# Performance work log

Measured on AMD Instinct MI355X. Metric: run time of the kernel, lower is better.

## Reference

```python
import jax, jax.numpy as jnp
import numpy as np

B, S, D, F, K = 32, 512, 256, 256, 3

def setup_inputs() -> dict:
    key = jax.random.key(0)
    ks = jax.random.split(key, 8)
    x = jax.random.normal(ks[0], (B, S, D), dtype=jnp.float32)
    target = jax.random.uniform(ks[1], (B, S), dtype=jnp.float32, minval=1.0, maxval=8.0)
    expand_max_len = int(jnp.round(target.sum(-1)).max())
    sc = 0.05
    conv1_w = jax.random.normal(ks[2], (F, D, K), dtype=jnp.float32) * sc
    conv1_b = jnp.zeros((F,), jnp.float32)
    conv2_w = jax.random.normal(ks[3], (F, F, K), dtype=jnp.float32) * sc
    conv2_b = jnp.zeros((F,), jnp.float32)
    norm1_g = jnp.ones((F,), jnp.float32); norm1_b = jnp.zeros((F,), jnp.float32)
    norm2_g = jnp.ones((F,), jnp.float32); norm2_b = jnp.zeros((F,), jnp.float32)
    lin_w = jax.random.normal(ks[4], (F,), dtype=jnp.float32) * sc
    lin_b = jnp.zeros((), jnp.float32)
    return {"x": x, "target": target, "conv1_w": conv1_w, "conv1_b": conv1_b,
            "conv2_w": conv2_w, "conv2_b": conv2_b, "norm1_g": norm1_g, "norm1_b": norm1_b,
            "norm2_g": norm2_g, "norm2_b": norm2_b, "lin_w": lin_w, "lin_b": lin_b,
            "expand_max_len": expand_max_len}

def _layernorm(h, g, b, eps=1e-5):
    mu = jnp.mean(h, axis=-1, keepdims=True)
    var = jnp.mean((h - mu) ** 2, axis=-1, keepdims=True)
    return (h - mu) * jax.lax.rsqrt(var + eps) * g + b

def _conv1d(h_bsd, w, bias):
    # h_bsd: [B,S,C] -> conv over time with 'same' padding -> [B,S,F]
    h = jnp.transpose(h_bsd, (0, 2, 1))  # [B,C,S]
    out = jax.lax.conv_general_dilated(h, w, window_strides=(1,),
                                       padding=[(K // 2, K // 2)],
                                       dimension_numbers=("NCH", "OIH", "NCH"))
    out = out + bias[None, :, None]
    return jnp.transpose(out, (0, 2, 1))  # [B,S,F]

def _duration_predict(x, conv1_w, conv1_b, conv2_w, conv2_b,
                      norm1_g, norm1_b, norm2_g, norm2_b, lin_w, lin_b):
    h = _conv1d(x, conv1_w, conv1_b)
    h = jax.nn.relu(_layernorm(h, norm1_g, norm1_b))  # dropout is identity in eval
    h = _conv1d(h, conv2_w, conv2_b)
    h = jax.nn.relu(_layernorm(h, norm2_g, norm2_b))
    return jax.nn.relu(h @ lin_w + lin_b)  # [B,S]

def _length_regulate(x, target, L):
    d = jnp.round(target)                # [B,S] integer-valued durations
    ends = jnp.cumsum(d, axis=-1)        # [B,S]
    starts = ends - d
    t = jnp.arange(L, dtype=d.dtype)     # [L]
    mask = ((t[None, None, :] >= starts[:, :, None]) &
            (t[None, None, :] < ends[:, :, None])).astype(x.dtype)  # [B,S,L]
    # x^T @ mask -> [B,D,L]; return transposed [B,L,D]
    return jnp.einsum("bsd,bsl->bld", x, mask)

def reference(x, target, conv1_w, conv1_b, conv2_w, conv2_b,
              norm1_g, norm1_b, norm2_g, norm2_b, lin_w, lin_b, expand_max_len):
    predicted_len = _duration_predict(x, conv1_w, conv1_b, conv2_w, conv2_b,
                                      norm1_g, norm1_b, norm2_g, norm2_b, lin_w, lin_b)
    output = _length_regulate(x, target, expand_max_len)
    return (output, predicted_len)
```

## Files before the change

### kernel.cpp

```cpp
#include <hip/hip_runtime.h>
#include <hip/hip_bf16.h>

#define NB 32
#define NS 512
#define NC 256
#define NKSTEP 24
#define ROWS 32
#define HALO_ROWS 34

typedef __attribute__((ext_vector_type(8))) short short8;
typedef __attribute__((ext_vector_type(4))) float f32x4;

__device__ __forceinline__ unsigned pack2(float a, float b) {
    __hip_bfloat16 ha = __float2bfloat16(a), hb = __float2bfloat16(b);
    return ((unsigned)(*(unsigned short*)&hb) << 16) | (unsigned)(*(unsigned short*)&ha);
}

__global__ __launch_bounds__(256) void prep_w(const float* __restrict__ w,
                                              unsigned short* __restrict__ Bp) {
    const int f = blockIdx.x, t = threadIdx.x;
    const float* wf = w + (size_t)f * 768 + t * 3;
    const float v[3] = {wf[0], wf[1], wf[2]};
#pragma unroll
    for (int shift = 0; shift < 3; ++shift) {
        const int k = shift * 256 + t;
        const int o = f * 32 + (k >> 5) * 8192 + (k & 31);
        __hip_bfloat16 h = __float2bfloat16(v[shift]);
        Bp[o] = *(unsigned short*)&h;
    }
}

template <bool FINAL, typename Tin>
__global__ __launch_bounds__(256, 2) void conv_mfma(
    const Tin* __restrict__ in,
    const uint4* __restrict__ Bp,
    const float* __restrict__ bias,
    const float* __restrict__ gamma,
    const float* __restrict__ beta,
    const float* __restrict__ linw,
    const float* __restrict__ linb,
    void* __restrict__ outp)
{
    __shared__ __align__(16) uint4 xs[HALO_ROWS * 32];
    __shared__ float red[ROWS][4][2];
    __shared__ float dotb[ROWS][4];

    const int tid = threadIdx.x;
    const int b   = blockIdx.x >> 4;
    const int s0  = (blockIdx.x & 15) << 5;

    {
        const int slot = tid & 31;
        for (int r = tid >> 5; r < HALO_ROWS; r += 8) {
            const int s = s0 - 1 + r;
            uint4 v = {0u, 0u, 0u, 0u};
            if (s >= 0 && s < NS) {
                if constexpr (sizeof(Tin) == 4) {
                    const float* src = (const float*)in + ((size_t)(b * NS + s)) * NC + slot * 8;
                    const float4 lo = *(const float4*)src;
                    const float4 hi = *(const float4*)(src + 4);
                    v.x = pack2(lo.x, lo.y); v.y = pack2(lo.z, lo.w);
                    v.z = pack2(hi.x, hi.y); v.w = pack2(hi.z, hi.w);
                } else {
                    v = *(const uint4*)((const unsigned short*)in +
                                        ((size_t)(b * NS + s)) * NC + slot * 8);
                }
            }
            xs[r * 32 + (slot ^ ((r & 7) << 2))] = v;
        }
    }
    __syncthreads();

    const int lane = tid & 63;
    const int w    = tid >> 6;
    const int n0   = w << 6;
    const int l15  = lane & 15;
    const int lg   = lane >> 4;

    f32x4 acc[2][4];
#pragma unroll
    for (int mi = 0; mi < 2; ++mi)
#pragma unroll
        for (int ni = 0; ni < 4; ++ni) acc[mi][ni] = (f32x4){0.f, 0.f, 0.f, 0.f};

    const uint4* bbase = Bp + (size_t)(n0 + l15) * 4 + lg;

    auto lda = [&](int ks, int mi) -> short8 {
        const int row  = mi * 16 + l15 + (ks >> 3);
        int slot = ((ks & 7) << 2) + lg;
        slot ^= (row & 7) << 2;
        return *(const short8*)&xs[row * 32 + slot];
    };
    auto ldb = [&](int ks, int ni) -> short8 {
        return *(const short8*)(const void*)(bbase + ks * 1024 + ni * 64);
    };

    short8 a0[2], b0[4], a1[2], b1[4];
#pragma unroll
    for (int mi = 0; mi < 2; ++mi) a0[mi] = lda(0, mi);
#pragma unroll
    for (int ni = 0; ni < 4; ++ni) b0[ni] = ldb(0, ni);

    for (int ks = 0; ks < NKSTEP; ks += 2) {
#pragma unroll
        for (int ni = 0; ni < 4; ++ni) b1[ni] = ldb(ks + 1, ni);
#pragma unroll
        for (int mi = 0; mi < 2; ++mi) a1[mi] = lda(ks + 1, mi);
#pragma unroll
        for (int mi = 0; mi < 2; ++mi)
#pragma unroll
            for (int ni = 0; ni < 4; ++ni)
                acc[mi][ni] = __builtin_amdgcn_mfma_f32_16x16x32_bf16(
                    a0[mi], b0[ni], acc[mi][ni], 0, 0, 0);
        if (ks + 2 < NKSTEP) {
#pragma unroll
            for (int ni = 0; ni < 4; ++ni) b0[ni] = ldb(ks + 2, ni);
#pragma unroll
            for (int mi = 0; mi < 2; ++mi) a0[mi] = lda(ks + 2, mi);
        }
#pragma unroll
        for (int mi = 0; mi < 2; ++mi)
#pragma unroll
            for (int ni = 0; ni < 4; ++ni)
                acc[mi][ni] = __builtin_amdgcn_mfma_f32_16x16x32_bf16(
                    a1[mi], b1[ni], acc[mi][ni], 0, 0, 0);
    }

    float bv[4], gv[4], bt[4], lwv[4];
#pragma unroll
    for (int ni = 0; ni < 4; ++ni) {
        const int col = n0 + ni * 16 + l15;
        bv[ni] = bias[col]; gv[ni] = gamma[col]; bt[ni] = beta[col];
        if constexpr (FINAL) lwv[ni] = linw[col];
    }
#pragma unroll
    for (int mi = 0; mi < 2; ++mi)
#pragma unroll
        for (int ni = 0; ni < 4; ++ni)
#pragma unroll
            for (int i = 0; i < 4; ++i) acc[mi][ni][i] += bv[ni];

#pragma unroll
    for (int mi = 0; mi < 2; ++mi) {
        float s[4] = {0, 0, 0, 0}, q[4] = {0, 0, 0, 0};
#pragma unroll
        for (int ni = 0; ni < 4; ++ni)
#pragma unroll
            for (int i = 0; i < 4; ++i) {
                const float v = acc[mi][ni][i];
                s[i] += v; q[i] += v * v;
            }
#pragma unroll
        for (int i = 0; i < 4; ++i)
#pragma unroll
            for (int m = 1; m < 16; m <<= 1) {
                s[i] += __shfl_xor(s[i], m, 64);
                q[i] += __shfl_xor(q[i], m, 64);
            }
        if (l15 == 0) {
#pragma unroll
            for (int i = 0; i < 4; ++i) {
                red[mi * 16 + lg * 4 + i][w][0] = s[i];
                red[mi * 16 + lg * 4 + i][w][1] = q[i];
            }
        }
    }
    __syncthreads();

#pragma unroll
    for (int mi = 0; mi < 2; ++mi) {
#pragma unroll
        for (int i = 0; i < 4; ++i) {
            const int row = mi * 16 + lg * 4 + i;
            float sum = 0.f, sq = 0.f;
#pragma unroll
            for (int ww = 0; ww < 4; ++ww) { sum += red[row][ww][0]; sq += red[row][ww][1]; }
            const float mu = sum * (1.f / 256.f);
            const float rs = rsqrtf(sq * (1.f / 256.f) - mu * mu + 1e-5f);
            float p = 0.f;
#pragma unroll
            for (int ni = 0; ni < 4; ++ni) {
                const float y = fmaxf(0.f, (acc[mi][ni][i] - mu) * rs * gv[ni] + bt[ni]);
                if constexpr (!FINAL) {
                    __hip_bfloat16 h = __float2bfloat16(y);
                    ((unsigned short*)outp)[((size_t)(b * NS + s0 + row)) * NC +
                                            n0 + ni * 16 + l15] = *(unsigned short*)&h;
                } else {
                    p += y * lwv[ni];
                }
            }
            if constexpr (FINAL) {
#pragma unroll
                for (int m = 1; m < 16; m <<= 1) p += __shfl_xor(p, m, 64);
                if (l15 == 0) dotb[row][w] = p;
            }
        }
    }
    if constexpr (FINAL) {
        __syncthreads();
        if (tid < ROWS) {
            const float tot = dotb[tid][0] + dotb[tid][1] + dotb[tid][2] + dotb[tid][3] + linb[0];
            ((float*)outp)[b * NS + s0 + tid] = fmaxf(0.f, tot);
        }
    }
}

__global__ __launch_bounds__(256) void scan_kernel(const float* __restrict__ target,
                                                   float* __restrict__ ends)
{
    __shared__ float bufa[512], bufb[512];
    const int b = blockIdx.x, t = threadIdx.x;
    const float* tb = target + (size_t)b * NS;
    bufa[t]       = rintf(tb[t]);
    bufa[t + 256] = rintf(tb[t + 256]);
    __syncthreads();
    float* src = bufa;
    float* dst = bufb;
    for (int off = 1; off < 512; off <<= 1) {
        for (int i = t; i < 512; i += 256) {
            float v = src[i];
            if (i >= off) v += src[i - off];
            dst[i] = v;
        }
        __syncthreads();
        float* tmp = src; src = dst; dst = tmp;
    }
    ends[(size_t)b * NS + t]       = src[t];
    ends[(size_t)b * NS + t + 256] = src[t + 256];
}

__global__ __launch_bounds__(256) void gather_kernel(const float* __restrict__ x,
                                                     const float* __restrict__ ends,
                                                     float* __restrict__ out, int L)
{
    const int b   = blockIdx.y;
    const int t0  = blockIdx.x * 8;
    const int tid = threadIdx.x;
    const float* eb = ends + (size_t)b * NS;
    const float total = eb[511];
    for (int i = 0; i < 8; ++i) {
        const int t = t0 + i;
        if (t >= L) return;
        const float tf = (float)t;
        float v = 0.f;
        if (tf < total) {
            int pos = 0;
#pragma unroll
            for (int st = 256; st > 0; st >>= 1)
                if (eb[pos + st - 1] <= tf) pos += st;
            v = x[((size_t)(b * NS + pos)) * NC + tid];
        }
        out[((size_t)b * L + t) * NC + tid] = v;
    }
}

extern "C" void kernel_launch(void* const* d_in, const int* in_sizes, int n_in,
                              void* d_out, int out_size, void* d_ws, size_t ws_size,
                              hipStream_t stream)
{
    const float* x    = (const float*)d_in[0];
    const float* targ = (const float*)d_in[1];
    const float* c1w  = (const float*)d_in[2];
    const float* c1b  = (const float*)d_in[3];
    const float* c2w  = (const float*)d_in[4];
    const float* c2b  = (const float*)d_in[5];
    const float* n1g  = (const float*)d_in[6];
    const float* n1b  = (const float*)d_in[7];
    const float* n2g  = (const float*)d_in[8];
    const float* n2b  = (const float*)d_in[9];
    const float* lw   = (const float*)d_in[10];
    const float* lb   = (const float*)d_in[11];

    const int L = (out_size - NB * NS) / (NB * NC);

    unsigned short* Bp1 = (unsigned short*)d_ws;
    unsigned short* Bp2 = Bp1 + 196608;
    unsigned short* h1  = Bp2 + 196608;
    float* ends = (float*)(h1 + (size_t)NB * NS * NC);
    float* out  = (float*)d_out;
    float* pred = out + (size_t)NB * (size_t)L * NC;

    prep_w<<<dim3(256), 256, 0, stream>>>(c1w, Bp1);
    prep_w<<<dim3(256), 256, 0, stream>>>(c2w, Bp2);

    conv_mfma<false, float><<<dim3(NB * 16), 256, 0, stream>>>(
        x, (const uint4*)Bp1, c1b, n1g, n1b, nullptr, nullptr, (void*)h1);
    conv_mfma<true, unsigned short><<<dim3(NB * 16), 256, 0, stream>>>(
        h1, (const uint4*)Bp2, c2b, n2g, n2b, lw, lb, (void*)pred);

    scan_kernel<<<dim3(NB), 256, 0, stream>>>(targ, ends);
    gather_kernel<<<dim3((L + 7) / 8, NB), 256, 0, stream>>>(x, ends, out, L);
}
```

Before: 185.2 us.

## Merge weight prep, deepen MFMA prefetch, scatter frame indices for float4 gather

Combines the two weight-prep launches into one grid. Fully unrolls the conv K loop with a 4-deep B-register and 2-deep A-register prefetch ring. Replaces the per-frame binary search gather with a scan that scatters a per-frame source index, followed by a float4-vectorized gather. This cuts launch count, global-load latency stalls, and the search cost in the memory-bound length-regulation step, at the cost of more registers and an extra index buffer pass.

```diff
diff --git a/kernel.cpp b/kernel.cpp
--- a/kernel.cpp
+++ b/kernel.cpp
@@ -16,9 +16,14 @@
     return ((unsigned)(*(unsigned short*)&hb) << 16) | (unsigned)(*(unsigned short*)&ha);
 }
 
-__global__ __launch_bounds__(256) void prep_w(const float* __restrict__ w,
-                                              unsigned short* __restrict__ Bp) {
-    const int f = blockIdx.x, t = threadIdx.x;
+__global__ __launch_bounds__(256) void prep_w2(const float* __restrict__ w1,
+                                               const float* __restrict__ w2,
+                                               unsigned short* __restrict__ Bp1,
+                                               unsigned short* __restrict__ Bp2) {
+    const bool second = blockIdx.x >= 256;
+    const int f = blockIdx.x & 255, t = threadIdx.x;
+    const float* w = second ? w2 : w1;
+    unsigned short* Bp = second ? Bp2 : Bp1;
     const float* wf = w + (size_t)f * 768 + t * 3;
     const float v[3] = {wf[0], wf[1], wf[2]};
 #pragma unroll
@@ -95,35 +100,33 @@
         return *(const short8*)(const void*)(bbase + ks * 1024 + ni * 64);
     };
 
-    short8 a0[2], b0[4], a1[2], b1[4];
-#pragma unroll
-    for (int mi = 0; mi < 2; ++mi) a0[mi] = lda(0, mi);
-#pragma unroll
-    for (int ni = 0; ni < 4; ++ni) b0[ni] = ldb(0, ni);
-
-    for (int ks = 0; ks < NKSTEP; ks += 2) {
-#pragma unroll
-        for (int ni = 0; ni < 4; ++ni) b1[ni] = ldb(ks + 1, ni);
-#pragma unroll
-        for (int mi = 0; mi < 2; ++mi) a1[mi] = lda(ks + 1, mi);
+    short8 areg[2][2], breg[4][4];
+#pragma unroll
+    for (int q = 0; q < 4; ++q)
+#pragma unroll
+        for (int ni = 0; ni < 4; ++ni) breg[q][ni] = ldb(q, ni);
+#pragma unroll
+    for (int p = 0; p < 2; ++p)
+#pragma unroll
+        for (int mi = 0; mi < 2; ++mi) areg[p][mi] = lda(p, mi);
+
+#pragma unroll
+    for (int p = 0; p < NKSTEP; ++p) {
+        const int bs = p & 3, as = p & 1;
 #pragma unroll
         for (int mi = 0; mi < 2; ++mi)
 #pragma unroll
             for (int ni = 0; ni < 4; ++ni)
                 acc[mi][ni] = __builtin_amdgcn_mfma_f32_16x16x32_bf16(
-                    a0[mi], b0[ni], acc[mi][ni], 0, 0, 0);
-        if (ks + 2 < NKSTEP) {
-#pragma unroll
-            for (int ni = 0; ni < 4; ++ni) b0[ni] = ldb(ks + 2, ni);
-#pragma unroll
-            for (int mi = 0; mi < 2; ++mi) a0[mi] = lda(ks + 2, mi);
-        }
-#pragma unroll
-        for (int mi = 0; mi < 2; ++mi)
-#pragma unroll
-            for (int ni = 0; ni < 4; ++ni)
-                acc[mi][ni] = __builtin_amdgcn_mfma_f32_16x16x32_bf16(
-                    a1[mi], b1[ni], acc[mi][ni], 0, 0, 0);
+                    areg[as][mi], breg[bs][ni], acc[mi][ni], 0, 0, 0);
+        if (p + 4 < NKSTEP) {
+#pragma unroll
+            for (int ni = 0; ni < 4; ++ni) breg[bs][ni] = ldb(p + 4, ni);
+        }
+        if (p + 2 < NKSTEP) {
+#pragma unroll
+            for (int mi = 0; mi < 2; ++mi) areg[as][mi] = lda(p + 2, mi);
+        }
     }
 
     float bv[4], gv[4], bt[4], lwv[4];
@@ -205,53 +208,46 @@
     }
 }
 
-__global__ __launch_bounds__(256) void scan_kernel(const float* __restrict__ target,
-                                                   float* __restrict__ ends)
-{
-    __shared__ float bufa[512], bufb[512];
+__global__ __launch_bounds__(256) void scan_scatter(const float* __restrict__ target,
+                                                    int* __restrict__ idx, int L)
+{
+    __shared__ int bufa[512], bufb[512];
     const int b = blockIdx.x, t = threadIdx.x;
     const float* tb = target + (size_t)b * NS;
-    bufa[t]       = rintf(tb[t]);
-    bufa[t + 256] = rintf(tb[t + 256]);
+    const int d0 = (int)rintf(tb[t]);
+    const int d1 = (int)rintf(tb[t + 256]);
+    bufa[t] = d0; bufa[t + 256] = d1;
     __syncthreads();
-    float* src = bufa;
-    float* dst = bufb;
+    int* src = bufa;
+    int* dst = bufb;
     for (int off = 1; off < 512; off <<= 1) {
         for (int i = t; i < 512; i += 256) {
-            float v = src[i];
+            int v = src[i];
             if (i >= off) v += src[i - off];
             dst[i] = v;
         }
         __syncthreads();
-        float* tmp = src; src = dst; dst = tmp;
-    }
-    ends[(size_t)b * NS + t]       = src[t];
-    ends[(size_t)b * NS + t + 256] = src[t + 256];
-}
-
-__global__ __launch_bounds__(256) void gather_kernel(const float* __restrict__ x,
-                                                     const float* __restrict__ ends,
-                                                     float* __restrict__ out, int L)
-{
-    const int b   = blockIdx.y;
-    const int t0  = blockIdx.x * 8;
-    const int tid = threadIdx.x;
-    const float* eb = ends + (size_t)b * NS;
-    const float total = eb[511];
-    for (int i = 0; i < 8; ++i) {
-        const int t = t0 + i;
-        if (t >= L) return;
-        const float tf = (float)t;
-        float v = 0.f;
-        if (tf < total) {
-            int pos = 0;
-#pragma unroll
-            for (int st = 256; st > 0; st >>= 1)
-                if (eb[pos + st - 1] <= tf) pos += st;
-            v = x[((size_t)(b * NS + pos)) * NC + tid];
-        }
-        out[((size_t)b * L + t) * NC + tid] = v;
-    }
+        int* tmp = src; src = dst; dst = tmp;
+    }
+    const int e0 = src[t], e1 = src[t + 256], total = src[511];
+    int* ib = idx + (size_t)b * L;
+    for (int k = e0 - d0; k < e0; ++k) ib[k] = t;
+    for (int k = e1 - d1; k < e1; ++k) ib[k] = t + 256;
+    for (int k = total + t; k < L; k += 256) ib[k] = -1;
+}
+
+__global__ __launch_bounds__(256) void gather2(const float4* __restrict__ x4,
+                                               const int* __restrict__ idx,
+                                               float4* __restrict__ out4, int L)
+{
+    const int b     = blockIdx.y;
+    const int frame = blockIdx.x * 4 + (threadIdx.x >> 6);
+    const int lane  = threadIdx.x & 63;
+    if (frame >= L) return;
+    const int pos = idx[(size_t)b * L + frame];
+    float4 v = {0.f, 0.f, 0.f, 0.f};
+    if (pos >= 0) v = x4[(((size_t)(b * NS + pos)) << 6) + lane];
+    out4[(((size_t)b * L + frame) << 6) + lane] = v;
 }
 
 extern "C" void kernel_launch(void* const* d_in, const int* in_sizes, int n_in,
@@ -276,18 +272,18 @@
     unsigned short* Bp1 = (unsigned short*)d_ws;
     unsigned short* Bp2 = Bp1 + 196608;
     unsigned short* h1  = Bp2 + 196608;
-    float* ends = (float*)(h1 + (size_t)NB * NS * NC);
+    int* idx = (int*)(h1 + (size_t)NB * NS * NC);
     float* out  = (float*)d_out;
     float* pred = out + (size_t)NB * (size_t)L * NC;
 
-    prep_w<<<dim3(256), 256, 0, stream>>>(c1w, Bp1);
-    prep_w<<<dim3(256), 256, 0, stream>>>(c2w, Bp2);
+    prep_w2<<<dim3(512), 256, 0, stream>>>(c1w, c2w, Bp1, Bp2);
 
     conv_mfma<false, float><<<dim3(NB * 16), 256, 0, stream>>>(
         x, (const uint4*)Bp1, c1b, n1g, n1b, nullptr, nullptr, (void*)h1);
     conv_mfma<true, unsigned short><<<dim3(NB * 16), 256, 0, stream>>>(
         h1, (const uint4*)Bp2, c2b, n2g, n2b, lw, lb, (void*)pred);
 
-    scan_kernel<<<dim3(NB), 256, 0, stream>>>(targ, ends);
-    gather_kernel<<<dim3((L + 7) / 8, NB), 256, 0, stream>>>(x, ends, out, L);
-}
+    scan_scatter<<<dim3(NB), 256, 0, stream>>>(targ, idx, L);
+    gather2<<<dim3((L + 3) / 4, NB), 256, 0, stream>>>(
+        (const float4*)x, idx, (float4*)out, L);
+}
```

Result: faster. 162.0 us (-12.5%).
